# Kernel tuning notes

Hardware: AMD Instinct MI355X
Metric: run time of the kernel (lower is better)

The kernel has to match this reference:

```python
import jax, jax.numpy as jnp
import numpy as np

N_NODES = 50000
N_EDGES = 800000
D = 128


def setup_inputs() -> dict:
    key = jax.random.key(0)
    ks = jax.random.split(key, 8)
    # xavier-uniform bound for [D, D]
    bound = np.sqrt(6.0 / (D + D)).astype(np.float32)
    x = jax.random.normal(ks[0], (N_NODES, D), dtype=jnp.float32)
    edge_index = jax.random.randint(ks[1], (2, N_EDGES), 0, N_NODES)
    W0 = jax.random.uniform(ks[2], (D, D), jnp.float32, -bound, bound)
    W1 = jax.random.uniform(ks[3], (D, D), jnp.float32, -bound, bound)
    W2 = jax.random.uniform(ks[4], (D, D), jnp.float32, -bound, bound)
    b0 = jnp.zeros((D,), jnp.float32)
    b1 = jnp.zeros((D,), jnp.float32)
    b2 = jnp.zeros((D,), jnp.float32)
    return {"x": x, "edge_index": edge_index,
            "W0": W0, "b0": b0, "W1": W1, "b1": b1, "W2": W2, "b2": b2}


def _gcn_conv(h, W, b, row, col, norm, n):
    # PyG GCNConv: x' = hat(D)^-1/2 hat(A) hat(D)^-1/2 (h W) + b
    hw = h @ W                                   # [N, D]
    msg = norm[:, None] * hw[row]                # gather from source nodes
    agg = jax.ops.segment_sum(msg, col, num_segments=n)  # scatter-add to targets
    return agg + b


def reference(x, edge_index, W0, b0, W1, b1, W2, b2):
    n = x.shape[0]
    loops = jnp.arange(n)
    # add self-loops (PyG GCNConv default)
    row = jnp.concatenate([edge_index[0], loops])
    col = jnp.concatenate([edge_index[1], loops])
    deg = jax.ops.segment_sum(jnp.ones(row.shape, x.dtype), col, num_segments=n)
    dinv = jnp.where(deg > 0, jax.lax.rsqrt(deg), 0.0)
    norm = dinv[row] * dinv[col]
    # dropout omitted (eval/inference mode)
    res = []
    h = x
    for W, b in ((W0, b0), (W1, b1), (W2, b2)):
        h = jnp.tanh(_gcn_conv(h, W, b, row, col, norm, n))
        res.append(h)
    return jnp.stack(res, axis=1)  # [N, n_layers, D]
```

## Files before the change

### kernel.cpp

```cpp
#include <hip/hip_runtime.h>
#include <math.h>

#define N_NODES 50000
#define N_EDGES 800000
#define D 128
#define NPAD 50048
#define NBLK 196

typedef unsigned int uint32;

__device__ __forceinline__ ushort f2bf(float f) {
    uint32 u = __float_as_uint(f);
    u = (u + 0x7fff + ((u >> 16) & 1)) >> 16;
    return (ushort)u;
}
__device__ __forceinline__ float bf2f(ushort u) {
    return __uint_as_float(((uint32)u) << 16);
}


__global__ __launch_bounds__(256) void k_count(const int* __restrict__ col,
                                               int* __restrict__ counts,
                                               int* __restrict__ rank_buf) {
    int i4 = (blockIdx.x * 256 + threadIdx.x) * 4;
    if (i4 < N_EDGES) {
        int4 c = *(const int4*)(col + i4);
        int4 r;
        r.x = atomicAdd(&counts[c.x], 1);
        r.y = atomicAdd(&counts[c.y], 1);
        r.z = atomicAdd(&counts[c.z], 1);
        r.w = atomicAdd(&counts[c.w], 1);
        *(int4*)(rank_buf + i4) = r;
    }
}

__global__ __launch_bounds__(256) void k_scan_local(const int* __restrict__ counts,
                                                    int* __restrict__ offsets,
                                                    int* __restrict__ partials) {
    __shared__ int wsum[4];
    int tid = threadIdx.x;
    int i = blockIdx.x * 256 + tid;
    int v = (i < N_NODES) ? counts[i] : 0;
    int lane = tid & 63, wv = tid >> 6;
    int x = v;
    #pragma unroll
    for (int off = 1; off < 64; off <<= 1) {
        int y = __shfl_up(x, off);
        if (lane >= off) x += y;
    }
    if (lane == 63) wsum[wv] = x;
    __syncthreads();
    int b0 = wsum[0], b1 = wsum[1], b2 = wsum[2], b3 = wsum[3];
    int base = (wv > 0 ? b0 : 0) + (wv > 1 ? b1 : 0) + (wv > 2 ? b2 : 0);
    if (i < N_NODES) offsets[i] = base + x - v;
    if (tid == 255) partials[blockIdx.x] = b0 + b1 + b2 + b3;
}

__global__ __launch_bounds__(256) void k_scan_add(int* __restrict__ offsets,
                                                  const int* __restrict__ partials,
                                                  const int* __restrict__ counts,
                                                  float* __restrict__ dinv) {
    __shared__ int wsum[4];
    int tid = threadIdx.x;
    int p = (tid < (int)blockIdx.x && tid < NBLK) ? partials[tid] : 0;
    int lane = tid & 63, wv = tid >> 6;
    #pragma unroll
    for (int off = 32; off; off >>= 1) p += __shfl_down(p, off);
    if (lane == 0) wsum[wv] = p;
    __syncthreads();
    int base = wsum[0] + wsum[1] + wsum[2] + wsum[3];
    int i = blockIdx.x * 256 + tid;
    if (i < N_NODES) {
        offsets[i] += base;
        dinv[i] = rsqrtf((float)counts[i] + 1.0f);
    }
    if (i == 0) offsets[N_NODES] = N_EDGES;
}

__global__ __launch_bounds__(256) void k_fill(const int* __restrict__ row,
                                              const int* __restrict__ col,
                                              const int* __restrict__ offsets,
                                              const int* __restrict__ rank_buf,
                                              int* __restrict__ csr_rows) {
    int i4 = (blockIdx.x * 256 + threadIdx.x) * 4;
    if (i4 < N_EDGES) {
        int4 c = *(const int4*)(col + i4);
        int4 r = *(const int4*)(rank_buf + i4);
        int4 rw = *(const int4*)(row + i4);
        csr_rows[offsets[c.x] + r.x] = rw.x;
        csr_rows[offsets[c.y] + r.y] = rw.y;
        csr_rows[offsets[c.z] + r.z] = rw.z;
        csr_rows[offsets[c.w] + r.w] = rw.w;
    }
}

#define BM 32
#define NTILES ((N_NODES + BM - 1) / BM)
#define GEMM_BLOCKS 512

__global__ __launch_bounds__(256) void k_gemm(const float* __restrict__ h, int h_stride,
                                              const float* __restrict__ W,
                                              const float* __restrict__ dinv,
                                              ushort* __restrict__ hw) {
    __shared__ float Ws[D * D];
    __shared__ float hs[BM * D];
    int tid = threadIdx.x;

    const float4* W4 = (const float4*)W;
    float4* Ws4 = (float4*)Ws;
    #pragma unroll
    for (int i = 0; i < 16; ++i) Ws4[tid + 256 * i] = W4[tid + 256 * i];

    int tx = tid & 31;
    int ty = tid >> 5;
    float4* hs4 = (float4*)hs;

    for (int t = blockIdx.x; t < NTILES; t += GEMM_BLOCKS) {
        int row0 = t * BM;
        __syncthreads();
        #pragma unroll
        for (int i = 0; i < 4; ++i) {
            int idx = tid + 256 * i;
            int r = idx >> 5, c4 = idx & 31;
            int row = row0 + r;
            float4 v = make_float4(0.f, 0.f, 0.f, 0.f);
            if (row < N_NODES) v = *(const float4*)(h + (size_t)row * h_stride + c4 * 4);
            hs4[idx] = v;
        }
        __syncthreads();

        float acc[4][4] = {};
        for (int k = 0; k < D; k += 4) {
            float4 a[4], bv[4];
            #pragma unroll
            for (int i = 0; i < 4; ++i) a[i] = *(float4*)(hs + (4 * ty + i) * D + k);
            #pragma unroll
            for (int j = 0; j < 4; ++j) bv[j] = *(float4*)(Ws + (k + j) * D + 4 * tx);
            #pragma unroll
            for (int i = 0; i < 4; ++i) {
                float4 aa = a[i];
                acc[i][0] += aa.x * bv[0].x; acc[i][1] += aa.x * bv[0].y;
                acc[i][2] += aa.x * bv[0].z; acc[i][3] += aa.x * bv[0].w;
                acc[i][0] += aa.y * bv[1].x; acc[i][1] += aa.y * bv[1].y;
                acc[i][2] += aa.y * bv[1].z; acc[i][3] += aa.y * bv[1].w;
                acc[i][0] += aa.z * bv[2].x; acc[i][1] += aa.z * bv[2].y;
                acc[i][2] += aa.z * bv[2].z; acc[i][3] += aa.z * bv[2].w;
                acc[i][0] += aa.w * bv[3].x; acc[i][1] += aa.w * bv[3].y;
                acc[i][2] += aa.w * bv[3].z; acc[i][3] += aa.w * bv[3].w;
            }
        }
        #pragma unroll
        for (int i = 0; i < 4; ++i) {
            int row = row0 + 4 * ty + i;
            if (row < N_NODES) {
                float dr = dinv[row];
                ushort4 v;
                v.x = f2bf(acc[i][0] * dr);
                v.y = f2bf(acc[i][1] * dr);
                v.z = f2bf(acc[i][2] * dr);
                v.w = f2bf(acc[i][3] * dr);
                *((ushort4*)(hw + (size_t)row * D) + tx) = v;
            }
        }
    }
}

__global__ __launch_bounds__(256) void k_agg(const ushort* __restrict__ hw,
                                             const float* __restrict__ dinv,
                                             const int* __restrict__ offsets,
                                             const int* __restrict__ csr_rows,
                                             const float* __restrict__ bias,
                                             float* __restrict__ out, int layer) {
    int node = blockIdx.x * 4 + (threadIdx.x >> 6);
    int lane = threadIdx.x & 63;
    int h = lane >> 5;
    int ls = lane & 31;

    float4 acc = make_float4(0.f, 0.f, 0.f, 0.f);
    int s = offsets[node], e = offsets[node + 1];
    int j = s + h;
    for (; j + 6 < e; j += 8) {
        int r0 = csr_rows[j];
        int r1 = csr_rows[j + 2];
        int r2 = csr_rows[j + 4];
        int r3 = csr_rows[j + 6];
        ushort4 v0 = *((const ushort4*)(hw + (size_t)r0 * D) + ls);
        ushort4 v1 = *((const ushort4*)(hw + (size_t)r1 * D) + ls);
        ushort4 v2 = *((const ushort4*)(hw + (size_t)r2 * D) + ls);
        ushort4 v3 = *((const ushort4*)(hw + (size_t)r3 * D) + ls);
        acc.x += bf2f(v0.x) + bf2f(v1.x) + bf2f(v2.x) + bf2f(v3.x);
        acc.y += bf2f(v0.y) + bf2f(v1.y) + bf2f(v2.y) + bf2f(v3.y);
        acc.z += bf2f(v0.z) + bf2f(v1.z) + bf2f(v2.z) + bf2f(v3.z);
        acc.w += bf2f(v0.w) + bf2f(v1.w) + bf2f(v2.w) + bf2f(v3.w);
    }
    for (; j < e; j += 2) {
        int r = csr_rows[j];
        ushort4 v = *((const ushort4*)(hw + (size_t)r * D) + ls);
        acc.x += bf2f(v.x); acc.y += bf2f(v.y);
        acc.z += bf2f(v.z); acc.w += bf2f(v.w);
    }
    acc.x += __shfl_xor(acc.x, 32);
    acc.y += __shfl_xor(acc.y, 32);
    acc.z += __shfl_xor(acc.z, 32);
    acc.w += __shfl_xor(acc.w, 32);

    if (h == 0) {
        float di = dinv[node];
        ushort4 sv = *((const ushort4*)(hw + (size_t)node * D) + ls);
        float4 b = *((const float4*)bias + ls);
        float4 o;
        o.x = tanhf(di * (acc.x + bf2f(sv.x)) + b.x);
        o.y = tanhf(di * (acc.y + bf2f(sv.y)) + b.y);
        o.z = tanhf(di * (acc.z + bf2f(sv.z)) + b.z);
        o.w = tanhf(di * (acc.w + bf2f(sv.w)) + b.w);
        *((float4*)(out + ((size_t)node * 3 + layer) * D) + ls) = o;
    }
}


extern "C" void kernel_launch(void* const* d_in, const int* in_sizes, int n_in,
                              void* d_out, int out_size, void* d_ws, size_t ws_size,
                              hipStream_t stream) {
    const float* x  = (const float*)d_in[0];
    const int*   ei = (const int*)d_in[1];
    const float* W0 = (const float*)d_in[2];
    const float* b0 = (const float*)d_in[3];
    const float* W1 = (const float*)d_in[4];
    const float* b1 = (const float*)d_in[5];
    const float* W2 = (const float*)d_in[6];
    const float* b2 = (const float*)d_in[7];
    float* out = (float*)d_out;

    const int* row = ei;
    const int* col = ei + N_EDGES;

    float* dinv    = (float*)d_ws;
    int*   counts  = (int*)(dinv + NPAD);
    int*   offsets = counts + NPAD;
    int*   partials= offsets + NPAD;
    int*   rank_buf= partials + 256;
    int*   csr     = rank_buf + N_EDGES;
    ushort* hw     = (ushort*)(csr + N_EDGES);

    int nb_e4 = (N_EDGES / 4 + 255) / 256;

    hipMemsetAsync(counts, 0, NPAD * sizeof(int), stream);
    k_count<<<nb_e4, 256, 0, stream>>>(col, counts, rank_buf);
    k_scan_local<<<NBLK, 256, 0, stream>>>(counts, offsets, partials);
    k_scan_add<<<NBLK, 256, 0, stream>>>(offsets, partials, counts, dinv);
    k_fill<<<nb_e4, 256, 0, stream>>>(row, col, offsets, rank_buf, csr);

    int nb_agg = N_NODES / 4;

    const float* Ws_[3] = {W0, W1, W2};
    const float* bs_[3] = {b0, b1, b2};
    for (int l = 0; l < 3; ++l) {
        const float* h;
        int stride;
        if (l == 0) { h = x; stride = D; }
        else        { h = out + (size_t)(l - 1) * D; stride = 3 * D; }
        k_gemm<<<GEMM_BLOCKS, 256, 0, stream>>>(h, stride, Ws_[l], dinv, hw);
        k_agg<<<nb_agg, 256, 0, stream>>>(hw, dinv, offsets, csr, bs_[l], out, l);
    }
}
```

Measured before the change: 355.7 us.

## Use bf16 MFMA for the feature GEMM and feed it bf16 activations

Replaces the scalar fp32 shared-memory GEMM with bf16 MFMA 16x16x32 instructions, using a padded transposed bf16 copy of W in LDS and 64-row tiles. The aggregation kernel also writes a bf16 copy of each layer's output so the next GEMM reads half the bytes instead of re-reading the strided fp32 output. Results are staged through LDS so global stores are coalesced. Inputs are rounded to bf16 before multiplication, which lowers precision relative to the fp32 GEMM.

After: 309.0 us. 1.15x faster.

```diff
diff --git a/kernel.cpp b/kernel.cpp
--- a/kernel.cpp
+++ b/kernel.cpp
@@ -8,6 +8,8 @@
 #define NBLK 196
 
 typedef unsigned int uint32;
+typedef __attribute__((ext_vector_type(8))) short short8;
+typedef __attribute__((ext_vector_type(4))) float f32x4;
 
 __device__ __forceinline__ ushort f2bf(float f) {
     uint32 u = __float_as_uint(f);
@@ -94,72 +96,104 @@
     }
 }
 
-#define BM 32
+#define BM 64
+#define LDA 136
 #define NTILES ((N_NODES + BM - 1) / BM)
 #define GEMM_BLOCKS 512
 
-__global__ __launch_bounds__(256) void k_gemm(const float* __restrict__ h, int h_stride,
+__global__ __launch_bounds__(256) void k_gemm(const float* __restrict__ hf,
+                                              const ushort* __restrict__ hb,
                                               const float* __restrict__ W,
                                               const float* __restrict__ dinv,
                                               ushort* __restrict__ hw) {
-    __shared__ float Ws[D * D];
-    __shared__ float hs[BM * D];
+    __shared__ __align__(16) ushort As[BM * LDA];
+    __shared__ __align__(16) ushort Wt[D * LDA];
     int tid = threadIdx.x;
-
-    const float4* W4 = (const float4*)W;
-    float4* Ws4 = (float4*)Ws;
-    #pragma unroll
-    for (int i = 0; i < 16; ++i) Ws4[tid + 256 * i] = W4[tid + 256 * i];
-
-    int tx = tid & 31;
-    int ty = tid >> 5;
-    float4* hs4 = (float4*)hs;
+    int lane = tid & 63;
+    int w = tid >> 6;
+    int quad = lane >> 4;
+    int m16 = lane & 15;
+
+    #pragma unroll 4
+    for (int i = 0; i < 64; ++i) {
+        int flat = tid + 256 * i;
+        int k = flat >> 7, n = flat & 127;
+        Wt[n * LDA + k] = f2bf(W[flat]);
+    }
 
     for (int t = blockIdx.x; t < NTILES; t += GEMM_BLOCKS) {
         int row0 = t * BM;
         __syncthreads();
+
+        {
+            int base = tid * 32;
+            int r = base >> 7, c = base & 127;
+            int row = row0 + r;
+            ushort* dst = As + r * LDA + c;
+            if (hf) {
+                if (row < N_NODES) {
+                    const float4* src = (const float4*)(hf + (size_t)row * D + c);
+                    #pragma unroll
+                    for (int j = 0; j < 4; ++j) {
+                        float4 v0 = src[2 * j], v1 = src[2 * j + 1];
+                        ushort4 u0, u1;
+                        u0.x = f2bf(v0.x); u0.y = f2bf(v0.y); u0.z = f2bf(v0.z); u0.w = f2bf(v0.w);
+                        u1.x = f2bf(v1.x); u1.y = f2bf(v1.y); u1.z = f2bf(v1.z); u1.w = f2bf(v1.w);
+                        *(ushort4*)(dst + 8 * j) = u0;
+                        *(ushort4*)(dst + 8 * j + 4) = u1;
+                    }
+                } else {
+                    short8 z = {};
+                    #pragma unroll
+                    for (int j = 0; j < 4; ++j) *(short8*)(dst + 8 * j) = z;
+                }
+            } else {
+                if (row < N_NODES) {
+                    const short8* src = (const short8*)(hb + (size_t)row * D + c);
+                    #pragma unroll
+                    for (int j = 0; j < 4; ++j) *(short8*)(dst + 8 * j) = src[j];
+                } else {
+                    short8 z = {};
+                    #pragma unroll
+                    for (int j = 0; j < 4; ++j) *(short8*)(dst + 8 * j) = z;
+                }
+            }
+        }
+        __syncthreads();
+
+        f32x4 acc[8];
+        #pragma unroll
+        for (int ct = 0; ct < 8; ++ct) acc[ct] = (f32x4){0.f, 0.f, 0.f, 0.f};
+        #pragma unroll
+        for (int ks = 0; ks < 4; ++ks) {
+            short8 a = *(const short8*)(As + (w * 16 + m16) * LDA + ks * 32 + quad * 8);
+            #pragma unroll
+            for (int ct = 0; ct < 8; ++ct) {
+                short8 b = *(const short8*)(Wt + (ct * 16 + m16) * LDA + ks * 32 + quad * 8);
+                acc[ct] = __builtin_amdgcn_mfma_f32_16x16x32_bf16(a, b, acc[ct], 0, 0, 0);
+            }
+        }
+
+        float dv[4];
+        #pragma unroll
+        for (int r = 0; r < 4; ++r) {
+            int row = row0 + w * 16 + quad * 4 + r;
+            dv[r] = (row < N_NODES) ? dinv[row] : 0.f;
+        }
+        #pragma unroll
+        for (int ct = 0; ct < 8; ++ct) {
+            #pragma unroll
+            for (int r = 0; r < 4; ++r)
+                As[(w * 16 + quad * 4 + r) * LDA + ct * 16 + m16] = f2bf(acc[ct][r] * dv[r]);
+        }
         #pragma unroll
         for (int i = 0; i < 4; ++i) {
-            int idx = tid + 256 * i;
-            int r = idx >> 5, c4 = idx & 31;
-            int row = row0 + r;
-            float4 v = make_float4(0.f, 0.f, 0.f, 0.f);
-            if (row < N_NODES) v = *(const float4*)(h + (size_t)row * h_stride + c4 * 4);
-            hs4[idx] = v;
-        }
-        __syncthreads();
-
-        float acc[4][4] = {};
-        for (int k = 0; k < D; k += 4) {
-            float4 a[4], bv[4];
-            #pragma unroll
-            for (int i = 0; i < 4; ++i) a[i] = *(float4*)(hs + (4 * ty + i) * D + k);
-            #pragma unroll
-            for (int j = 0; j < 4; ++j) bv[j] = *(float4*)(Ws + (k + j) * D + 4 * tx);
-            #pragma unroll
-            for (int i = 0; i < 4; ++i) {
-                float4 aa = a[i];
-                acc[i][0] += aa.x * bv[0].x; acc[i][1] += aa.x * bv[0].y;
-                acc[i][2] += aa.x * bv[0].z; acc[i][3] += aa.x * bv[0].w;
-                acc[i][0] += aa.y * bv[1].x; acc[i][1] += aa.y * bv[1].y;
-                acc[i][2] += aa.y * bv[1].z; acc[i][3] += aa.y * bv[1].w;
-                acc[i][0] += aa.z * bv[2].x; acc[i][1] += aa.z * bv[2].y;
-                acc[i][2] += aa.z * bv[2].z; acc[i][3] += aa.z * bv[2].w;
-                acc[i][0] += aa.w * bv[3].x; acc[i][1] += aa.w * bv[3].y;
-                acc[i][2] += aa.w * bv[3].z; acc[i][3] += aa.w * bv[3].w;
-            }
-        }
-        #pragma unroll
-        for (int i = 0; i < 4; ++i) {
-            int row = row0 + 4 * ty + i;
+            int chunk = i * 64 + lane;
+            int r = chunk >> 4, c8 = chunk & 15;
+            int row = row0 + w * 16 + r;
             if (row < N_NODES) {
-                float dr = dinv[row];
-                ushort4 v;
-                v.x = f2bf(acc[i][0] * dr);
-                v.y = f2bf(acc[i][1] * dr);
-                v.z = f2bf(acc[i][2] * dr);
-                v.w = f2bf(acc[i][3] * dr);
-                *((ushort4*)(hw + (size_t)row * D) + tx) = v;
+                short8 v = *(const short8*)(As + (w * 16 + r) * LDA + c8 * 8);
+                *(short8*)(hw + (size_t)row * D + c8 * 8) = v;
             }
         }
     }
@@ -170,7 +204,8 @@
                                              const int* __restrict__ offsets,
                                              const int* __restrict__ csr_rows,
                                              const float* __restrict__ bias,
-                                             float* __restrict__ out, int layer) {
+                                             float* __restrict__ out, int layer,
+                                             ushort* __restrict__ hnext, int write_next) {
     int node = blockIdx.x * 4 + (threadIdx.x >> 6);
     int lane = threadIdx.x & 63;
     int h = lane >> 5;
@@ -214,6 +249,11 @@
         o.z = tanhf(di * (acc.z + bf2f(sv.z)) + b.z);
         o.w = tanhf(di * (acc.w + bf2f(sv.w)) + b.w);
         *((float4*)(out + ((size_t)node * 3 + layer) * D) + ls) = o;
+        if (write_next) {
+            ushort4 nv;
+            nv.x = f2bf(o.x); nv.y = f2bf(o.y); nv.z = f2bf(o.z); nv.w = f2bf(o.w);
+            *((ushort4*)(hnext + (size_t)node * D) + ls) = nv;
+        }
     }
 }
 
@@ -241,6 +281,7 @@
     int*   rank_buf= partials + 256;
     int*   csr     = rank_buf + N_EDGES;
     ushort* hw     = (ushort*)(csr + N_EDGES);
+    ushort* hnext  = hw + (size_t)NPAD * D;
 
     int nb_e4 = (N_EDGES / 4 + 255) / 256;
 
@@ -255,11 +296,9 @@
     const float* Ws_[3] = {W0, W1, W2};
     const float* bs_[3] = {b0, b1, b2};
     for (int l = 0; l < 3; ++l) {
-        const float* h;
-        int stride;
-        if (l == 0) { h = x; stride = D; }
-        else        { h = out + (size_t)(l - 1) * D; stride = 3 * D; }
-        k_gemm<<<GEMM_BLOCKS, 256, 0, stream>>>(h, stride, Ws_[l], dinv, hw);
-        k_agg<<<nb_agg, 256, 0, stream>>>(hw, dinv, offsets, csr, bs_[l], out, l);
-    }
-}
+        if (l == 0) k_gemm<<<GEMM_BLOCKS, 256, 0, stream>>>(x, (const ushort*)nullptr, Ws_[l], dinv, hw);
+        else        k_gemm<<<GEMM_BLOCKS, 256, 0, stream>>>((const float*)nullptr, hnext, Ws_[l], dinv, hw);
+        k_agg<<<nb_agg, 256, 0, stream>>>(hw, dinv, offsets, csr, bs_[l], out, l,
+                                          hnext, l < 2 ? 1 : 0);
+    }
+}
```
